# Performance work log

Measured on AMD Instinct MI355X. Metric: run time of the kernel, lower is better.

## Reference

```python
import jax, jax.numpy as jnp
import numpy as np
from jax import lax

NUM_CLASSES = 5
CONF_THRESH = 0.6
NMS_THRESH = 0.2
NUM_TOPK = 64          # min(topk=1000, 64) as in post_process
STRIDES = (8, 16, 32)
FMP = ((160, 160), (80, 80), (40, 40))  # 1280x1280 input
BATCH = 128


def setup_inputs() -> dict:
    key = jax.random.key(0)
    ks = jax.random.split(key, 9)
    d = {}
    i = 0
    for name, (h, w) in zip(("8", "16", "32"), FMP):
        hw = h * w
        d["obj" + name] = jax.random.normal(ks[i], (BATCH, hw, 1), jnp.float32); i += 1
        d["cls" + name] = jax.random.normal(ks[i], (BATCH, hw, NUM_CLASSES), jnp.float32); i += 1
        d["reg" + name] = jax.random.normal(ks[i], (BATCH, hw, 4), jnp.float32); i += 1
    return d


def make_anchors(h, w, stride):
    ay, ax = jnp.meshgrid(jnp.arange(h), jnp.arange(w), indexing="ij")
    xy = jnp.stack([ax, ay], axis=-1).astype(jnp.float32).reshape(-1, 2)
    return (xy + 0.5) * stride  # [HW, 2]


def decode_boxes(reg, anchors, stride):
    # ctr = reg[:, :2]*stride + anchor;  wh = exp(reg[:, 2:])*stride
    ctr = reg[:, :2] * stride + anchors
    wh = jnp.exp(reg[:, 2:]) * stride
    return jnp.concatenate([ctr - 0.5 * wh, ctr + 0.5 * wh], axis=-1)  # x1y1x2y2


def iou_matrix(b):
    # Faithful to YOLO.nms: areas un-clamped, intersection w/h clamped at 1e-10
    x1, y1, x2, y2 = b[:, 0], b[:, 1], b[:, 2], b[:, 3]
    areas = (x2 - x1) * (y2 - y1)
    xx1 = jnp.maximum(x1[:, None], x1[None, :])
    yy1 = jnp.maximum(y1[:, None], y1[None, :])
    xx2 = jnp.minimum(x2[:, None], x2[None, :])
    yy2 = jnp.minimum(y2[:, None], y2[None, :])
    w = jnp.maximum(1e-10, xx2 - xx1)
    h = jnp.maximum(1e-10, yy2 - yy1)
    inter = w * h
    return inter / (areas[:, None] + areas[None, :] - inter)


def nms_keep(iou, valid):
    # Greedy NMS on score-sorted candidates: fixed-length sequential suppression.
    n = iou.shape[0]
    idx = jnp.arange(n)
    def body(i, keep):
        sup = keep[i] & (iou[i] > NMS_THRESH) & (idx > i)
        return keep & jnp.logical_not(sup)
    return lax.fori_loop(0, n, body, valid)


def _single_image(obj8, cls8, reg8, obj16, cls16, reg16, obj32, cls32, reg32):
    levels = ((obj8, cls8, reg8), (obj16, cls16, reg16), (obj32, cls32, reg32))
    sc, lb, bx, vd = [], [], [], []
    for lvl, (obj, cls, reg) in enumerate(levels):
        h, w = FMP[lvl]
        s = STRIDES[lvl]
        anchors = make_anchors(h, w, s)
        boxes = decode_boxes(reg, anchors, s)                      # [HW, 4]
        scores = jnp.sqrt(jax.nn.sigmoid(obj) * jax.nn.sigmoid(cls)).reshape(-1)  # [HW*C]
        top_s, top_i = lax.top_k(scores, NUM_TOPK)
        a_idx = top_i // NUM_CLASSES
        labels = top_i % NUM_CLASSES
        sc.append(top_s)
        lb.append(labels)
        bx.append(boxes[a_idx])
        vd.append(top_s > CONF_THRESH)
    scores = jnp.concatenate(sc)          # [192]
    labels = jnp.concatenate(lb)
    boxes = jnp.concatenate(bx)           # [192, 4]
    valid = jnp.concatenate(vd)
    # Global score order (within each class this matches the per-class argsort)
    order = jnp.argsort(-scores)
    scores, labels, boxes, valid = scores[order], labels[order], boxes[order], valid[order]
    # Class-offset trick: boxes of different classes have IoU ~ 0 -> exactly per-class NMS
    off = labels.astype(jnp.float32) * (2.0 * jnp.max(jnp.abs(boxes)) + 1.0)
    keep = nms_keep(iou_matrix(boxes + off[:, None]), valid)
    scores = jnp.where(keep, scores, 0.0)
    boxes = jnp.where(keep[:, None], boxes, 0.0)
    labels = jnp.where(keep, labels, -1)
    return boxes, scores, labels


def reference(obj8, cls8, reg8, obj16, cls16, reg16, obj32, cls32, reg32):
    # Batched (vmapped) version of inference_single_image's decode+postprocess.
    # Returns fixed-size masked outputs: boxes [B,192,4], scores [B,192], labels [B,192].
    return jax.vmap(_single_image)(obj8, cls8, reg8, obj16, cls16, reg16, obj32, cls32, reg32)
```

## Files before the change

### kernel.cpp

```cpp
#include <hip/hip_runtime.h>


#define NUM_CLASSES 5
#define CONF_THRESH 0.6f
#define NMS_THRESH  0.2f
#define TOPK   64
#define BATCH  128
#define TOTK   192
#define NCH    21
#define CHUNK  1600
#define SCAP   2048
#define SOFT   768

typedef unsigned long long u64;
typedef unsigned int u32;

__device__ void bitonic_desc(u64* k, int m) {
  for (int kk = 2; kk <= m; kk <<= 1) {
    for (int j = kk >> 1; j > 0; j >>= 1) {
      __syncthreads();
      for (int i = threadIdx.x; i < m; i += blockDim.x) {
        int ixj = i ^ j;
        if (ixj > i) {
          u64 a = k[i], b = k[ixj];
          bool sw = ((i & kk) == 0) ? (a < b) : (a > b);
          if (sw) { k[i] = b; k[ixj] = a; }
        }
      }
    }
  }
  __syncthreads();
}

__device__ inline u64 wave_sort64_desc(u64 v, int lane) {
  #pragma unroll
  for (int k = 2; k <= 64; k <<= 1) {
    #pragma unroll
    for (int j = k >> 1; j > 0; j >>= 1) {
      u64 o = __shfl_xor(v, j, 64);
      bool keepMax = (((lane & k) == 0) != ((lane & j) != 0));
      v = keepMax ? (v > o ? v : o) : (v < o ? v : o);
    }
  }
  return v;
}

__device__ __forceinline__ u64 u64max(u64 a, u64 b) { return a > b ? a : b; }
__device__ __forceinline__ u64 u64min(u64 a, u64 b) { return a < b ? a : b; }

__device__ __forceinline__ u64 bmerge64_desc(u64 v, int lane) {
  #pragma unroll
  for (int j = 32; j > 0; j >>= 1) {
    u64 o = __shfl_xor(v, j, 64);
    v = ((lane & j) == 0) ? u64max(v, o) : u64min(v, o);
  }
  return v;
}

__device__ __forceinline__ u64 merge_top64(u64 a, u64 brev, int lane) {
  return bmerge64_desc(u64max(a, brev), lane);
}

__device__ __forceinline__ u64 merge4_top64(u64 a, u64 brev, u64 c, u64 drev, int lane) {
  u64 ab = merge_top64(a, brev, lane);
  u64 cd = merge_top64(c, drev, lane);
  u64 cdr = __shfl(cd, 63 - lane, 64);
  return merge_top64(ab, cdr, lane);
}

__device__ inline u64 score_key(float so, float cv, int idx) {
  float sc = 1.0f / (1.0f + expf(-cv));
  float s  = sqrtf(__fmul_rn(so, sc));
  return ((u64)__float_as_uint(s) << 32) | (u32)(~(u32)idx);
}

__device__ inline float sigmoidf(float x) { return 1.0f / (1.0f + expf(-x)); }

__global__ __launch_bounds__(256) void scan_kernel(
    const float* __restrict__ obj8,  const float* __restrict__ cls8,
    const float* __restrict__ obj16, const float* __restrict__ cls16,
    const float* __restrict__ obj32, const float* __restrict__ cls32,
    u64* __restrict__ ws_part) {
  __shared__ u64 keys[SCAP];
  __shared__ int cnt;
  __shared__ u64 sthr[4];

  const int bx  = blockIdx.x;
  const int img = bx / NCH;
  const int c   = bx - img * NCH;
  const int t   = threadIdx.x;
  const int lane = t & 63, wv = t >> 6;

  const float *obj, *cls;
  int hw, off;
  if (c < 16)      { obj = obj8;  cls = cls8;  hw = 25600; off = c * CHUNK; }
  else if (c < 20) { obj = obj16; cls = cls16; hw = 6400;  off = (c - 16) * CHUNK; }
  else             { obj = obj32; cls = cls32; hw = 1600;  off = 0; }
  obj += (size_t)img * hw + off;
  cls += ((size_t)img * hw + off) * NUM_CLASSES;

  u64 kk[20];
  u64 mx;
  {
    const float4* c4 = (const float4*)cls + (size_t)t * 5;
    float4 q0 = c4[0], q1 = c4[1], q2 = c4[2], q3 = c4[3], q4 = c4[4];
    float4 ov = ((const float4*)obj)[t];
    float cv[20] = { q0.x,q0.y,q0.z,q0.w, q1.x,q1.y,q1.z,q1.w,
                     q2.x,q2.y,q2.z,q2.w, q3.x,q3.y,q3.z,q3.w,
                     q4.x,q4.y,q4.z,q4.w };
    float os[4] = { sigmoidf(ov.x), sigmoidf(ov.y), sigmoidf(ov.z), sigmoidf(ov.w) };
    int ga0 = off + 4 * t;
    #pragma unroll
    for (int a = 0; a < 4; ++a)
      #pragma unroll
      for (int j = 0; j < 5; ++j)
        kk[a * 5 + j] = score_key(os[a], cv[a * 5 + j], (ga0 + a) * NUM_CLASSES + j);
    mx = kk[0];
    #pragma unroll
    for (int i = 1; i < 20; ++i) if (kk[i] > mx) mx = kk[i];
  }
  u64 srt = wave_sort64_desc(mx, lane);
  if (lane == 15) sthr[wv] = srt;
  if (t == 0) cnt = 0;
  __syncthreads();
  u64 thr;
  {
    u64 a0 = sthr[0], a1 = sthr[1], a2 = sthr[2], a3 = sthr[3];
    u64 mn = a0 < a1 ? a0 : a1;
    u64 mn2 = a2 < a3 ? a2 : a3;
    thr = (mn < mn2 ? mn : mn2) - 1ull;
  }

  int cs = 0;
  #pragma unroll
  for (int a = 0; a < 4; ++a) {
    #pragma unroll
    for (int j = 0; j < 5; ++j) {
      u64 key = kk[a * 5 + j];
      if (key > thr) { int p = atomicAdd(&cnt, 1); if (p < SCAP) keys[p] = key; }
    }
    __syncthreads();
    cs = cnt;
    __syncthreads();
    if (cs > SOFT) {
      int m = 64; while (m < cs) m <<= 1;
      for (int i = cs + t; i < m; i += 256) keys[i] = 0ull;
      bitonic_desc(keys, m);
      if (t == 0) cnt = TOPK;
      u64 nt = keys[TOPK - 1];
      __syncthreads();
      thr = nt; cs = TOPK;
    }
  }

  const bool act2 = (t < 144);
  if (act2) {
    const float4* c4 = (const float4*)cls + 1280 + (size_t)t * 5;
    float4 q0 = c4[0], q1 = c4[1], q2 = c4[2], q3 = c4[3], q4 = c4[4];
    float4 ov = ((const float4*)obj)[256 + t];
    float cv[20] = { q0.x,q0.y,q0.z,q0.w, q1.x,q1.y,q1.z,q1.w,
                     q2.x,q2.y,q2.z,q2.w, q3.x,q3.y,q3.z,q3.w,
                     q4.x,q4.y,q4.z,q4.w };
    float os[4] = { sigmoidf(ov.x), sigmoidf(ov.y), sigmoidf(ov.z), sigmoidf(ov.w) };
    int ga0 = off + 1024 + 4 * t;
    #pragma unroll
    for (int a = 0; a < 4; ++a)
      #pragma unroll
      for (int j = 0; j < 5; ++j)
        kk[a * 5 + j] = score_key(os[a], cv[a * 5 + j], (ga0 + a) * NUM_CLASSES + j);
  }
  #pragma unroll
  for (int a = 0; a < 4; ++a) {
    if (act2) {
      #pragma unroll
      for (int j = 0; j < 5; ++j) {
        u64 key = kk[a * 5 + j];
        if (key > thr) { int p = atomicAdd(&cnt, 1); if (p < SCAP) keys[p] = key; }
      }
    }
    __syncthreads();
    cs = cnt;
    __syncthreads();
    if (cs > SOFT) {
      int m = 64; while (m < cs) m <<= 1;
      for (int i = cs + t; i < m; i += 256) keys[i] = 0ull;
      bitonic_desc(keys, m);
      if (t == 0) cnt = TOPK;
      u64 nt = keys[TOPK - 1];
      __syncthreads();
      thr = nt; cs = TOPK;
    }
  }

  {
    int m = 64; while (m < cs) m <<= 1;
    for (int i = cs + t; i < m; i += 256) keys[i] = 0ull;
    bitonic_desc(keys, m);
  }
  if (t < TOPK) ws_part[(size_t)bx * TOPK + t] = keys[t];
}

__global__ __launch_bounds__(256) void merge_nms_kernel(
    const u64* __restrict__ ws_part,
    const float* __restrict__ reg8, const float* __restrict__ reg16, const float* __restrict__ reg32,
    float* __restrict__ out) {
  __shared__ u64   lds_runs[256];
  __shared__ u64   lvlkeys[TOTK];
  __shared__ u64   skeys[TOTK];
  __shared__ int   slb[TOTK];
  __shared__ float sbx[TOTK * 4];
  __shared__ float sX1[TOTK], sY1[TOTK], sX2[TOTK], sY2[TOTK], sA[TOTK];
  __shared__ u64   rows[TOTK * 3];
  __shared__ u64   svalid[3];
  __shared__ u64   skeep[3];
  __shared__ float lmarr[3];

  const int img  = blockIdx.x;
  const int t    = threadIdx.x;
  const int lane = t & 63, wv = t >> 6;

  const u64* pbase = ws_part + (size_t)img * NCH * TOPK;

  {
    const u64* q = pbase + (size_t)(4 * wv) * TOPK;
    u64 a    = q[lane];
    u64 brev = q[64 + 63 - lane];
    u64 c    = q[128 + lane];
    u64 drev = q[192 + 63 - lane];
    lds_runs[wv * 64 + lane] = merge4_top64(a, brev, c, drev, lane);
    if (wv == 3) lvlkeys[128 + lane] = pbase[20 * TOPK + lane];
  }
  __syncthreads();

  if (wv == 0) {
    u64 a    = lds_runs[lane];
    u64 brev = lds_runs[64 + 63 - lane];
    u64 c    = lds_runs[128 + lane];
    u64 drev = lds_runs[192 + 63 - lane];
    lvlkeys[lane] = merge4_top64(a, brev, c, drev, lane);
  } else if (wv == 1) {
    const u64* q = pbase + (size_t)16 * TOPK;
    u64 a    = q[lane];
    u64 brev = q[64 + 63 - lane];
    u64 c    = q[128 + lane];
    u64 drev = q[192 + 63 - lane];
    lvlkeys[64 + lane] = merge4_top64(a, brev, c, drev, lane);
  }
  __syncthreads();

  if (wv == 0) {
    const u64 HIMASK = 0xFFFFFFFF00000000ull;
    u64 s0 = (lvlkeys[lane] & HIMASK) | (u32)(~(u32)lane);
    int i1 = 64 + 63 - lane;
    u64 s1r = (lvlkeys[i1] & HIMASK) | (u32)(~(u32)i1);
    int i2 = 128 + 63 - lane;
    u64 s2r = (lvlkeys[i2] & HIMASK) | (u32)(~(u32)i2);
    u64 hi_ = bmerge64_desc(u64max(s0, s1r), lane);
    u64 lo_ = bmerge64_desc(u64min(s0, s1r), lane);
    u64 R1   = u64max(lo_, s2r);
    u64 out0 = bmerge64_desc(u64max(hi_, R1), lane);
    u64 out1 = bmerge64_desc(u64min(hi_, R1), lane);
    u64 out2 = bmerge64_desc(u64min(lo_, s2r), lane);
    skeys[lane]       = out0;
    skeys[64 + lane]  = out1;
    skeys[128 + lane] = out2;
  } else {
    int idx = t - 64;
    const float* reg; int w; int hw; float stride;
    if (wv == 1)      { reg = reg8;  w = 160; hw = 25600; stride = 8.0f;  }
    else if (wv == 2) { reg = reg16; w = 80;  hw = 6400;  stride = 16.0f; }
    else              { reg = reg32; w = 40;  hw = 1600;  stride = 32.0f; }
    reg += (size_t)img * hw * 4;
    u64 key = lvlkeys[idx];
    u32 raw = ~((u32)key);
    int a = (int)(raw / NUM_CLASSES);
    int c = (int)(raw - (u32)a * NUM_CLASSES);
    int ix = a % w, iy = a / w;
    float ax = __fmul_rn((float)ix + 0.5f, stride);
    float ay = __fmul_rn((float)iy + 0.5f, stride);
    float r0 = reg[a*4+0], r1 = reg[a*4+1], r2 = reg[a*4+2], r3 = reg[a*4+3];
    float cx = __fadd_rn(__fmul_rn(r0, stride), ax);
    float cy = __fadd_rn(__fmul_rn(r1, stride), ay);
    float wd = __fmul_rn(expf(r2), stride);
    float ht = __fmul_rn(expf(r3), stride);
    float x1 = __fsub_rn(cx, __fmul_rn(0.5f, wd));
    float y1 = __fsub_rn(cy, __fmul_rn(0.5f, ht));
    float x2 = __fadd_rn(cx, __fmul_rn(0.5f, wd));
    float y2 = __fadd_rn(cy, __fmul_rn(0.5f, ht));
    slb[idx] = c;
    sbx[idx*4+0] = x1; sbx[idx*4+1] = y1;
    sbx[idx*4+2] = x2; sbx[idx*4+3] = y2;
  }
  __syncthreads();

  float sc_r = 0.0f, b0 = 0.0f, b1 = 0.0f, b2 = 0.0f, b3 = 0.0f;
  int p = 0, lb_r = 0;
  if (t < TOTK) {
    u64 key = skeys[t];
    p = (int)(~((u32)key)) & 255;
    sc_r = __uint_as_float((u32)(key >> 32));
    lb_r = slb[p];
    b0 = sbx[p*4+0]; b1 = sbx[p*4+1]; b2 = sbx[p*4+2]; b3 = sbx[p*4+3];
    float lm = fmaxf(fmaxf(fabsf(b0), fabsf(b1)), fmaxf(fabsf(b2), fabsf(b3)));
    #pragma unroll
    for (int d = 32; d > 0; d >>= 1) lm = fmaxf(lm, __shfl_xor(lm, d, 64));
    if (lane == 0) lmarr[wv] = lm;
  }
  __syncthreads();

  const float lmAll = fmaxf(fmaxf(lmarr[0], lmarr[1]), lmarr[2]);
  const float offscale = __fadd_rn(__fmul_rn(2.0f, lmAll), 1.0f);

  float X1 = 0.0f, Y1 = 0.0f, X2 = 0.0f, Y2 = 0.0f, A = 0.0f;
  if (t < TOTK) {
    float off = __fmul_rn((float)lb_r, offscale);
    X1 = __fadd_rn(b0, off); Y1 = __fadd_rn(b1, off);
    X2 = __fadd_rn(b2, off); Y2 = __fadd_rn(b3, off);
    A  = __fmul_rn(__fsub_rn(X2, X1), __fsub_rn(Y2, Y1));
    sX1[t] = X1; sY1[t] = Y1; sX2[t] = X2; sY2[t] = Y2; sA[t] = A;
    u64 bal = __ballot(sc_r > CONF_THRESH);
    if (lane == 0) svalid[wv] = bal;
  }
  __syncthreads();

  if (t < TOTK) {
    u64 r0m = 0, r1m = 0, r2m = 0;
    for (int j = t + 1; j < TOTK; ++j) {
      float xx1 = fmaxf(X1, sX1[j]);
      float yy1 = fmaxf(Y1, sY1[j]);
      float xx2 = fminf(X2, sX2[j]);
      float yy2 = fminf(Y2, sY2[j]);
      float wv2 = fmaxf(1e-10f, __fsub_rn(xx2, xx1));
      float hv = fmaxf(1e-10f, __fsub_rn(yy2, yy1));
      float inter = __fmul_rn(wv2, hv);
      float den = __fsub_rn(__fadd_rn(A, sA[j]), inter);
      float iou = __fdiv_rn(inter, den);
      if (iou > NMS_THRESH) {
        u64 b = 1ull << (j & 63);
        int wd = j >> 6;
        r0m |= (wd == 0) ? b : 0ull;
        r1m |= (wd == 1) ? b : 0ull;
        r2m |= (wd == 2) ? b : 0ull;
      }
    }
    rows[t*3+0] = r0m; rows[t*3+1] = r1m; rows[t*3+2] = r2m;
  }
  __syncthreads();

  if (t < 64) {
    u64 k0 = svalid[0], k1 = svalid[1], k2 = svalid[2];
    #pragma unroll 4
    for (int i = 0; i < 64; ++i) {
      u64 m0 = rows[i*3+0], m1 = rows[i*3+1], m2 = rows[i*3+2];
      u64 sel = 0ull - ((k0 >> i) & 1ull);
      k0 &= ~(m0 & sel); k1 &= ~(m1 & sel); k2 &= ~(m2 & sel);
    }
    #pragma unroll 4
    for (int i = 0; i < 64; ++i) {
      int r = 64 + i;
      u64 m0 = rows[r*3+0], m1 = rows[r*3+1], m2 = rows[r*3+2];
      u64 sel = 0ull - ((k1 >> i) & 1ull);
      k0 &= ~(m0 & sel); k1 &= ~(m1 & sel); k2 &= ~(m2 & sel);
    }
    #pragma unroll 4
    for (int i = 0; i < 64; ++i) {
      int r = 128 + i;
      u64 m0 = rows[r*3+0], m1 = rows[r*3+1], m2 = rows[r*3+2];
      u64 sel = 0ull - ((k2 >> i) & 1ull);
      k0 &= ~(m0 & sel); k1 &= ~(m1 & sel); k2 &= ~(m2 & sel);
    }
    if (t == 0) { skeep[0] = k0; skeep[1] = k1; skeep[2] = k2; }
  }
  __syncthreads();

  if (t < TOTK) {
    float* out_boxes  = out;
    float* out_scores = out + (size_t)BATCH * TOTK * 4;
    float* out_labels = out + (size_t)BATCH * TOTK * 5;
    bool kp = (skeep[t >> 6] >> (t & 63)) & 1ull;
    int gi = img * TOTK + t;
    out_boxes[gi*4+0] = kp ? sbx[p*4+0] : 0.0f;
    out_boxes[gi*4+1] = kp ? sbx[p*4+1] : 0.0f;
    out_boxes[gi*4+2] = kp ? sbx[p*4+2] : 0.0f;
    out_boxes[gi*4+3] = kp ? sbx[p*4+3] : 0.0f;
    out_scores[gi] = kp ? sc_r : 0.0f;
    out_labels[gi] = kp ? (float)lb_r : -1.0f;
  }
}

extern "C" void kernel_launch(void* const* d_in, const int* in_sizes, int n_in,
                              void* d_out, int out_size, void* d_ws, size_t ws_size,
                              hipStream_t stream) {
  const float* obj8  = (const float*)d_in[0];
  const float* cls8  = (const float*)d_in[1];
  const float* reg8  = (const float*)d_in[2];
  const float* obj16 = (const float*)d_in[3];
  const float* cls16 = (const float*)d_in[4];
  const float* reg16 = (const float*)d_in[5];
  const float* obj32 = (const float*)d_in[6];
  const float* cls32 = (const float*)d_in[7];
  const float* reg32 = (const float*)d_in[8];

  u64* ws_part = (u64*)d_ws;

  scan_kernel<<<dim3(BATCH * NCH), dim3(256), 0, stream>>>(
      obj8, cls8, obj16, cls16, obj32, cls32, ws_part);
  merge_nms_kernel<<<dim3(BATCH), dim3(256), 0, stream>>>(
      ws_part, reg8, reg16, reg32, (float*)d_out);
}
```

Baseline: 243.8 us.

## Prefilter scan candidates with cheap reciprocal score product before exact key computation

The scan kernel now computes a cheap proxy (1+e^-o)(1+e^-c) with fast exp for every anchor-class pair. It derives a conservative threshold from a per-wave 64-way sort of per-thread minima, then pushes only passing candidates to an LDS worklist, where the exact sigmoid/sqrt key is recomputed from reloaded inputs. Block size changes from 256 to 320 threads so each thread covers 5 anchors, and the soft cap before re-sorting drops from 768 to 448. This avoids most exact key computations and 64-bit compares, at the cost of a second global reload for survivors and reliance on the approximate prefilter margin for correctness.

```diff
diff --git a/kernel.cpp b/kernel.cpp
--- a/kernel.cpp
+++ b/kernel.cpp
@@ -10,7 +10,9 @@
 #define NCH    21
 #define CHUNK  1600
 #define SCAP   2048
-#define SOFT   768
+#define SOFT   448
+#define NTHR   320
+#define WCAP   1600
 
 typedef unsigned long long u64;
 typedef unsigned int u32;
@@ -32,12 +34,12 @@
   __syncthreads();
 }
 
-__device__ inline u64 wave_sort64_desc(u64 v, int lane) {
+__device__ inline u32 wave_sort64_desc_u32(u32 v, int lane) {
   #pragma unroll
   for (int k = 2; k <= 64; k <<= 1) {
     #pragma unroll
     for (int j = k >> 1; j > 0; j >>= 1) {
-      u64 o = __shfl_xor(v, j, 64);
+      u32 o = __shfl_xor(v, j, 64);
       bool keepMax = (((lane & k) == 0) != ((lane & j) != 0));
       v = keepMax ? (v > o ? v : o) : (v < o ? v : o);
     }
@@ -76,14 +78,16 @@
 
 __device__ inline float sigmoidf(float x) { return 1.0f / (1.0f + expf(-x)); }
 
-__global__ __launch_bounds__(256) void scan_kernel(
+__global__ __launch_bounds__(NTHR) void scan_kernel(
     const float* __restrict__ obj8,  const float* __restrict__ cls8,
     const float* __restrict__ obj16, const float* __restrict__ cls16,
     const float* __restrict__ obj32, const float* __restrict__ cls32,
     u64* __restrict__ ws_part) {
   __shared__ u64 keys[SCAP];
+  __shared__ u32 wl[WCAP];
   __shared__ int cnt;
-  __shared__ u64 sthr[4];
+  __shared__ int wcnt;
+  __shared__ u32 sthr[5];
 
   const int bx  = blockIdx.x;
   const int img = bx / NCH;
@@ -99,102 +103,79 @@
   obj += (size_t)img * hw + off;
   cls += ((size_t)img * hw + off) * NUM_CLASSES;
 
-  u64 kk[20];
-  u64 mx;
+  float ff[25];
   {
-    const float4* c4 = (const float4*)cls + (size_t)t * 5;
-    float4 q0 = c4[0], q1 = c4[1], q2 = c4[2], q3 = c4[3], q4 = c4[4];
-    float4 ov = ((const float4*)obj)[t];
-    float cv[20] = { q0.x,q0.y,q0.z,q0.w, q1.x,q1.y,q1.z,q1.w,
-                     q2.x,q2.y,q2.z,q2.w, q3.x,q3.y,q3.z,q3.w,
-                     q4.x,q4.y,q4.z,q4.w };
-    float os[4] = { sigmoidf(ov.x), sigmoidf(ov.y), sigmoidf(ov.z), sigmoidf(ov.w) };
-    int ga0 = off + 4 * t;
     #pragma unroll
-    for (int a = 0; a < 4; ++a)
+    for (int a = 0; a < 5; ++a) {
+      float o = obj[a * NTHR + t];
+      float dob = 1.0f + __expf(-o);
       #pragma unroll
-      for (int j = 0; j < 5; ++j)
-        kk[a * 5 + j] = score_key(os[a], cv[a * 5 + j], (ga0 + a) * NUM_CLASSES + j);
-    mx = kk[0];
-    #pragma unroll
-    for (int i = 1; i < 20; ++i) if (kk[i] > mx) mx = kk[i];
-  }
-  u64 srt = wave_sort64_desc(mx, lane);
-  if (lane == 15) sthr[wv] = srt;
-  if (t == 0) cnt = 0;
-  __syncthreads();
-  u64 thr;
+      for (int j = 0; j < 5; ++j) {
+        float cvv = cls[(a * NTHR + t) * 5 + j];
+        ff[a * 5 + j] = dob * (1.0f + __expf(-cvv));
+      }
+    }
+  }
+  float pmin = ff[0];
+  #pragma unroll
+  for (int i = 1; i < 25; ++i) pmin = fminf(pmin, ff[i]);
+  u32 srt = wave_sort64_desc_u32(__float_as_uint(pmin), lane);
+  if (lane == 48) sthr[wv] = srt;
+  if (t == 0) { cnt = 0; wcnt = 0; }
+  __syncthreads();
+  u64 thr; float thr_inv;
   {
-    u64 a0 = sthr[0], a1 = sthr[1], a2 = sthr[2], a3 = sthr[3];
-    u64 mn = a0 < a1 ? a0 : a1;
-    u64 mn2 = a2 < a3 ? a2 : a3;
-    thr = (mn < mn2 ? mn : mn2) - 1ull;
+    float pmax = __uint_as_float(sthr[0]);
+    pmax = fmaxf(pmax, __uint_as_float(sthr[1]));
+    pmax = fmaxf(pmax, __uint_as_float(sthr[2]));
+    pmax = fmaxf(pmax, __uint_as_float(sthr[3]));
+    pmax = fmaxf(pmax, __uint_as_float(sthr[4]));
+    float ts = sqrtf(__fdiv_rn(1.0f, pmax)) * (1.0f - 1e-4f);
+    thr = ((u64)__float_as_uint(ts) << 32) - 1ull;
+    thr_inv = __fdiv_rn(1.0f, __fmul_rn(__fmul_rn(ts, ts), 1.0f - 2e-4f));
   }
 
   int cs = 0;
   #pragma unroll
-  for (int a = 0; a < 4; ++a) {
+  for (int a = 0; a < 5; ++a) {
     #pragma unroll
     for (int j = 0; j < 5; ++j) {
-      u64 key = kk[a * 5 + j];
+      if (ff[a * 5 + j] <= thr_inv) {
+        int p = atomicAdd(&wcnt, 1);
+        wl[p] = (u32)(((a * NTHR + t) << 3) | j);
+      }
+    }
+    __syncthreads();
+    int wc = wcnt;
+    for (int i = t; i < wc; i += NTHR) {
+      u32 cd = wl[i];
+      int al = (int)(cd >> 3);
+      int jj = (int)(cd & 7u);
+      float o   = obj[al];
+      float cvv = cls[al * 5 + jj];
+      u64 key = score_key(sigmoidf(o), cvv, (off + al) * NUM_CLASSES + jj);
       if (key > thr) { int p = atomicAdd(&cnt, 1); if (p < SCAP) keys[p] = key; }
     }
     __syncthreads();
+    if (t == 0) wcnt = 0;
     cs = cnt;
     __syncthreads();
     if (cs > SOFT) {
       int m = 64; while (m < cs) m <<= 1;
-      for (int i = cs + t; i < m; i += 256) keys[i] = 0ull;
+      for (int i = cs + t; i < m; i += NTHR) keys[i] = 0ull;
       bitonic_desc(keys, m);
       if (t == 0) cnt = TOPK;
       u64 nt = keys[TOPK - 1];
       __syncthreads();
       thr = nt; cs = TOPK;
-    }
-  }
-
-  const bool act2 = (t < 144);
-  if (act2) {
-    const float4* c4 = (const float4*)cls + 1280 + (size_t)t * 5;
-    float4 q0 = c4[0], q1 = c4[1], q2 = c4[2], q3 = c4[3], q4 = c4[4];
-    float4 ov = ((const float4*)obj)[256 + t];
-    float cv[20] = { q0.x,q0.y,q0.z,q0.w, q1.x,q1.y,q1.z,q1.w,
-                     q2.x,q2.y,q2.z,q2.w, q3.x,q3.y,q3.z,q3.w,
-                     q4.x,q4.y,q4.z,q4.w };
-    float os[4] = { sigmoidf(ov.x), sigmoidf(ov.y), sigmoidf(ov.z), sigmoidf(ov.w) };
-    int ga0 = off + 1024 + 4 * t;
-    #pragma unroll
-    for (int a = 0; a < 4; ++a)
-      #pragma unroll
-      for (int j = 0; j < 5; ++j)
-        kk[a * 5 + j] = score_key(os[a], cv[a * 5 + j], (ga0 + a) * NUM_CLASSES + j);
-  }
-  #pragma unroll
-  for (int a = 0; a < 4; ++a) {
-    if (act2) {
-      #pragma unroll
-      for (int j = 0; j < 5; ++j) {
-        u64 key = kk[a * 5 + j];
-        if (key > thr) { int p = atomicAdd(&cnt, 1); if (p < SCAP) keys[p] = key; }
-      }
-    }
-    __syncthreads();
-    cs = cnt;
-    __syncthreads();
-    if (cs > SOFT) {
-      int m = 64; while (m < cs) m <<= 1;
-      for (int i = cs + t; i < m; i += 256) keys[i] = 0ull;
-      bitonic_desc(keys, m);
-      if (t == 0) cnt = TOPK;
-      u64 nt = keys[TOPK - 1];
-      __syncthreads();
-      thr = nt; cs = TOPK;
+      float tsc = __uint_as_float((u32)(nt >> 32));
+      thr_inv = __fdiv_rn(1.0f, __fmul_rn(__fmul_rn(tsc, tsc), 1.0f - 2e-4f));
     }
   }
 
   {
     int m = 64; while (m < cs) m <<= 1;
-    for (int i = cs + t; i < m; i += 256) keys[i] = 0ull;
+    for (int i = cs + t; i < m; i += NTHR) keys[i] = 0ull;
     bitonic_desc(keys, m);
   }
   if (t < TOPK) ws_part[(size_t)bx * TOPK + t] = keys[t];
@@ -403,7 +384,7 @@
 
   u64* ws_part = (u64*)d_ws;
 
-  scan_kernel<<<dim3(BATCH * NCH), dim3(256), 0, stream>>>(
+  scan_kernel<<<dim3(BATCH * NCH), dim3(NTHR), 0, stream>>>(
       obj8, cls8, obj16, cls16, obj32, cls32, ws_part);
   merge_nms_kernel<<<dim3(BATCH), dim3(256), 0, stream>>>(
       ws_part, reg8, reg16, reg32, (float*)d_out);
```

Result: no change. 240.1 us (-1.5%).
